# Performance work log

Hardware: AMD Instinct MI355X
Metric: run time of the kernel (lower is better)

## Reference

```python
import jax, jax.numpy as jnp
import numpy as np

N_NODES = 50000
N_EDGES = 800000
IN_FT = 128
HID_FT = 64
EMB_FT = 128
NUM_LAYERS = 4
NEG_SLOP = 0.2


def setup_inputs() -> dict:
    key = jax.random.key(0)
    ks = jax.random.split(key, 16)
    x = jax.random.normal(ks[0], (N_NODES, IN_FT), dtype=jnp.float32)
    edge_index = jax.random.randint(ks[1], (2, N_EDGES), 0, N_NODES, dtype=jnp.int64)
    edge_weight = jax.random.uniform(ks[2], (N_EDGES,), dtype=jnp.float32)
    def lin(k, fin, fout):
        s = 1.0 / np.sqrt(fin)
        kw, kb = jax.random.split(k)
        W = jax.random.uniform(kw, (fin, fout), minval=-s, maxval=s, dtype=jnp.float32)
        b = jax.random.uniform(kb, (fout,), minval=-s, maxval=s, dtype=jnp.float32)
        return W, b
    W1, b1 = lin(ks[3], IN_FT, HID_FT)
    W2, b2 = lin(ks[4], HID_FT, HID_FT)
    W3, b3 = lin(ks[5], HID_FT, HID_FT)
    W4, b4 = lin(ks[6], HID_FT, HID_FT)
    Wh, bh = lin(ks[7], NUM_LAYERS * HID_FT, EMB_FT)
    return {"x": x, "edge_index": edge_index, "edge_weight": edge_weight,
            "W1": W1, "b1": b1, "W2": W2, "b2": b2, "W3": W3, "b3": b3,
            "W4": W4, "b4": b4, "Wh": Wh, "bh": bh}


def _gcn_no_norm(x, src, dst, ew, W, b):
    # GCNConv(add_self_loops=False, normalize=False): plain weighted scatter-add
    h = x @ W                                   # [N, F]
    msg = h[src] * ew[:, None]                  # gather over edges [E, F]
    return jax.ops.segment_sum(msg, dst, num_segments=N_NODES) + b


def _gcn_norm(x, src, dst, ew, W, b):
    # Default GCNConv: add self loops (weight 1) + symmetric normalization.
    deg = jax.ops.segment_sum(ew, dst, num_segments=N_NODES) + 1.0  # +1 self loop
    dinv = jnp.where(deg > 0, jax.lax.rsqrt(deg), 0.0)
    norm = dinv[src] * ew * dinv[dst]           # [E]
    h = x @ W
    agg = jax.ops.segment_sum(h[src] * norm[:, None], dst, num_segments=N_NODES)
    agg = agg + (dinv * dinv)[:, None] * h      # self-loop term
    return agg + b


def _forward(x, edge_index, edge_weight, W1, b1, W2, b2, W3, b3, W4, b4, Wh, bh):
    src, dst = edge_index[0], edge_index[1]
    lrelu = lambda v: jax.nn.leaky_relu(v, NEG_SLOP)
    outs = []
    h = lrelu(_gcn_no_norm(x, src, dst, edge_weight, W1, b1))
    outs.append(h)  # dropout is identity in deterministic reference
    for W, b in ((W2, b2), (W3, b3), (W4, b4)):
        h = lrelu(_gcn_norm(h, src, dst, edge_weight, W, b))
        outs.append(h)
    cat = jnp.concatenate(outs, axis=-1)        # [N, num_layers*HID_FT]
    return cat @ Wh + bh


def reference(x, edge_index, edge_weight, W1, b1, W2, b2, W3, b3, W4, b4, Wh, bh):
    return _forward(x, edge_index, edge_weight, W1, b1, W2, b2, W3, b3, W4, b4, Wh, bh)
```

## Files before the change

kernel.cpp:

```cpp
#include <hip/hip_runtime.h>
#include <hip/hip_bf16.h>

#define NEG_SLOP 0.2f
typedef unsigned long long ull;
typedef __attribute__((ext_vector_type(8))) short bf16x8;
typedef __attribute__((ext_vector_type(4))) float f32x4;

__device__ __forceinline__ float lrelu(float v) { return v > 0.0f ? v : NEG_SLOP * v; }

__device__ __forceinline__ float bf2f(unsigned short u) {
    union { unsigned int i; float f; } c; c.i = ((unsigned int)u) << 16; return c.f;
}
__device__ __forceinline__ unsigned short f2bf(float f) {
    union { float f; unsigned int i; } c; c.f = f;
    unsigned int r = c.i + 0x7FFF + ((c.i >> 16) & 1);
    return (unsigned short)(r >> 16);
}

struct us8 { ushort4 a, b; };

__global__ void prep_kernel(const float* __restrict__ Wh, unsigned short* __restrict__ wht,
                            const float* __restrict__ W1, unsigned short* __restrict__ w1t,
                            const float* __restrict__ W2, unsigned short* __restrict__ w2t,
                            const float* __restrict__ W3, unsigned short* __restrict__ w3t,
                            const float* __restrict__ W4, unsigned short* __restrict__ w4t,
                            float4* __restrict__ pz, int nz) {
    int idx = blockIdx.x * 256 + threadIdx.x;
    if (idx < nz) pz[idx] = make_float4(0.f, 0.f, 0.f, 0.f);
    if (idx < 256 * 128) {
        int k = idx >> 7, c = idx & 127;
        wht[(size_t)c * 256 + k] = f2bf(Wh[idx]);
    }
    if (idx < 64 * 128) {
        int c = idx >> 7, k = idx & 127;
        w1t[idx] = f2bf(W1[k * 64 + c]);
    }
    if (idx < 64 * 64) {
        int c = idx >> 6, k = idx & 63;
        w2t[idx] = f2bf(W2[k * 64 + c]);
        w3t[idx] = f2bf(W3[k * 64 + c]);
        w4t[idx] = f2bf(W4[k * 64 + c]);
    }
}

__global__ void histo_kernel(const int* __restrict__ dst, const float* __restrict__ ew,
                             ull* __restrict__ packed4, int* __restrict__ rank,
                             int n_edges, int n) {
    int e = blockIdx.x * 256 + threadIdx.x;
    if (e >= n_edges) return;
    int d = dst[e];
    int c = e & 3;
    ull delta = (1ULL << 40) | (ull)(ew[e] * 4294967296.0f);
    ull old = atomicAdd(&packed4[(size_t)c * n + d], delta);
    rank[e] = (int)(old >> 40);
}

__global__ void scan1_kernel(const ull* __restrict__ packed4, int* __restrict__ pre,
                             int4* __restrict__ bases, int* __restrict__ bsum,
                             float* __restrict__ dinv, int n) {
    __shared__ int s[256];
    int t = threadIdx.x;
    int base = blockIdx.x * 1024 + t * 4;
    const ull m = (1ULL << 40) - 1;
    int tot[4];
#pragma unroll
    for (int j = 0; j < 4; ++j) {
        int node = base + j;
        if (node < n) {
            ull p0 = packed4[node];
            ull p1 = packed4[(size_t)n + node];
            ull p2 = packed4[2 * (size_t)n + node];
            ull p3 = packed4[3 * (size_t)n + node];
            int c0 = (int)(p0 >> 40), c1 = (int)(p1 >> 40);
            int c2 = (int)(p2 >> 40), c3 = (int)(p3 >> 40);
            bases[node] = make_int4(0, c0, c0 + c1, c0 + c1 + c2);
            tot[j] = c0 + c1 + c2 + c3;
            float deg = (float)((p0 & m) + (p1 & m) + (p2 & m) + (p3 & m)) *
                        (1.0f / 4294967296.0f);
            dinv[node] = rsqrtf(deg + 1.0f);
        } else tot[j] = 0;
    }
    int tsum = tot[0] + tot[1] + tot[2] + tot[3];
    s[t] = tsum;
    __syncthreads();
    for (int off = 1; off < 256; off <<= 1) {
        int v = (t >= off) ? s[t - off] : 0;
        __syncthreads();
        s[t] += v;
        __syncthreads();
    }
    int ex = s[t] - tsum;
    if (t == 255) bsum[blockIdx.x] = s[255];
    int o[4];
    o[0] = ex; o[1] = ex + tot[0]; o[2] = o[1] + tot[1]; o[3] = o[2] + tot[2];
    if (base + 3 < n) *(int4*)&pre[base] = make_int4(o[0], o[1], o[2], o[3]);
    else {
        for (int j = 0; j < 4; ++j) if (base + j < n) pre[base + j] = o[j];
    }
}

__global__ void scan3_kernel(int* __restrict__ rp, int4* __restrict__ bases,
                             const int* __restrict__ bsum, int nbsum,
                             int n, int n_edges) {
    __shared__ int sb[64];
    __shared__ int boffs[64];
    int t = threadIdx.x;
    int myv = 0;
    if (t < 64) { myv = (t < nbsum) ? bsum[t] : 0; sb[t] = myv; }
    __syncthreads();
    for (int off = 1; off < 64; off <<= 1) {
        int u = (t >= off && t < 64) ? sb[t - off] : 0;
        __syncthreads();
        if (t < 64) sb[t] += u;
        __syncthreads();
    }
    if (t < 64) boffs[t] = sb[t] - myv;
    __syncthreads();
    int idx = blockIdx.x * 256 + t;
    int base = idx * 4;
    if (base >= n) {
        if (base == ((n + 3) & ~3)) rp[n] = n_edges;
        return;
    }
    int boff = boffs[(base >> 10) & 63];
    if (base + 3 < n) {
        int4 v = *(int4*)&rp[base];
        v.x += boff; v.y += boff; v.z += boff; v.w += boff;
        *(int4*)&rp[base] = v;
        int va[4] = {v.x, v.y, v.z, v.w};
#pragma unroll
        for (int j = 0; j < 4; ++j) {
            int4 bs = bases[base + j];
            bs.x += va[j]; bs.y += va[j]; bs.z += va[j]; bs.w += va[j];
            bases[base + j] = bs;
        }
    } else {
        for (int j = 0; j < 4 && base + j < n; ++j) {
            int v = rp[base + j] + boff;
            rp[base + j] = v;
            int4 bs = bases[base + j];
            bs.x += v; bs.y += v; bs.z += v; bs.w += v;
            bases[base + j] = bs;
        }
        rp[n] = n_edges;
    }
}

__global__ void fill_kernel(const int* __restrict__ src, const int* __restrict__ dst,
                            const float* __restrict__ ew, const int* __restrict__ rank,
                            const int4* __restrict__ bases,
                            int2* __restrict__ e_sw, int n_edges) {
    int e = blockIdx.x * 256 + threadIdx.x;
    if (e >= n_edges) return;
    int d = dst[e];
    int c = e & 3;
    int4 bs = bases[d];
    int b = (c == 0) ? bs.x : (c == 1) ? bs.y : (c == 2) ? bs.z : bs.w;
    e_sw[b + rank[e]] = make_int2(src[e], __float_as_int(ew[e]));
}

__global__ void gather_plain(const int* __restrict__ rp, const int2* __restrict__ e_sw,
                             const unsigned short* __restrict__ hb,
                             const float* __restrict__ b, unsigned short* __restrict__ cat, int n) {
    int node = (blockIdx.x * 256 + threadIdx.x) >> 6;
    if (node >= n) return;
    int lane = threadIdx.x & 63;
    int eg = lane >> 3;
    int f0 = (lane & 7) * 8;
    int lo = rp[node], hi = rp[node + 1];
    float a[8] = {};
    for (int k = lo + eg; k < hi; k += 16) {
        int k1 = k + 8;
        int2 p0 = e_sw[k];
        int2 p1 = e_sw[k1 < hi ? k1 : k];
        float w0 = __int_as_float(p0.y);
        float w1 = k1 < hi ? __int_as_float(p1.y) : 0.f;
        us8 u0 = *(const us8*)&hb[(size_t)p0.x * 64 + f0];
        us8 u1 = *(const us8*)&hb[(size_t)p1.x * 64 + f0];
        a[0] += w0 * bf2f(u0.a.x) + w1 * bf2f(u1.a.x);
        a[1] += w0 * bf2f(u0.a.y) + w1 * bf2f(u1.a.y);
        a[2] += w0 * bf2f(u0.a.z) + w1 * bf2f(u1.a.z);
        a[3] += w0 * bf2f(u0.a.w) + w1 * bf2f(u1.a.w);
        a[4] += w0 * bf2f(u0.b.x) + w1 * bf2f(u1.b.x);
        a[5] += w0 * bf2f(u0.b.y) + w1 * bf2f(u1.b.y);
        a[6] += w0 * bf2f(u0.b.z) + w1 * bf2f(u1.b.z);
        a[7] += w0 * bf2f(u0.b.w) + w1 * bf2f(u1.b.w);
    }
#pragma unroll
    for (int j = 0; j < 8; ++j) {
        a[j] += __shfl_xor(a[j], 8, 64);
        a[j] += __shfl_xor(a[j], 16, 64);
        a[j] += __shfl_xor(a[j], 32, 64);
    }
    if (eg == 0) {
        unsigned short o[8];
#pragma unroll
        for (int j = 0; j < 8; ++j) o[j] = f2bf(lrelu(a[j] + b[f0 + j]));
        *(int4*)&cat[(size_t)node * 256 + f0] = *(int4*)o;
    }
}

__global__ void gather_norm(const int* __restrict__ rp, const int2* __restrict__ e_sw,
                            const unsigned short* __restrict__ hb,
                            const float* __restrict__ dinv, const float* __restrict__ b,
                            unsigned short* __restrict__ cat, int col_off, int n) {
    int node = (blockIdx.x * 256 + threadIdx.x) >> 6;
    if (node >= n) return;
    int lane = threadIdx.x & 63;
    int eg = lane >> 3;
    int f0 = (lane & 7) * 8;
    float di = dinv[node];
    us8 h = *(const us8*)&hb[(size_t)node * 64 + f0];
    int lo = rp[node], hi = rp[node + 1];
    float a[8] = {};
    for (int k = lo + eg; k < hi; k += 16) {
        int k1 = k + 8;
        int2 p0 = e_sw[k];
        int2 p1 = e_sw[k1 < hi ? k1 : k];
        float w0 = __int_as_float(p0.y);
        float w1 = k1 < hi ? __int_as_float(p1.y) : 0.f;
        us8 u0 = *(const us8*)&hb[(size_t)p0.x * 64 + f0];
        us8 u1 = *(const us8*)&hb[(size_t)p1.x * 64 + f0];
        a[0] += w0 * bf2f(u0.a.x) + w1 * bf2f(u1.a.x);
        a[1] += w0 * bf2f(u0.a.y) + w1 * bf2f(u1.a.y);
        a[2] += w0 * bf2f(u0.a.z) + w1 * bf2f(u1.a.z);
        a[3] += w0 * bf2f(u0.a.w) + w1 * bf2f(u1.a.w);
        a[4] += w0 * bf2f(u0.b.x) + w1 * bf2f(u1.b.x);
        a[5] += w0 * bf2f(u0.b.y) + w1 * bf2f(u1.b.y);
        a[6] += w0 * bf2f(u0.b.z) + w1 * bf2f(u1.b.z);
        a[7] += w0 * bf2f(u0.b.w) + w1 * bf2f(u1.b.w);
    }
#pragma unroll
    for (int j = 0; j < 8; ++j) {
        a[j] += __shfl_xor(a[j], 8, 64);
        a[j] += __shfl_xor(a[j], 16, 64);
        a[j] += __shfl_xor(a[j], 32, 64);
    }
    if (eg == 0) {
        float hs[8] = {bf2f(h.a.x), bf2f(h.a.y), bf2f(h.a.z), bf2f(h.a.w),
                       bf2f(h.b.x), bf2f(h.b.y), bf2f(h.b.z), bf2f(h.b.w)};
        unsigned short o[8];
#pragma unroll
        for (int j = 0; j < 8; ++j) o[j] = f2bf(lrelu(di * (a[j] + hs[j]) + b[f0 + j]));
        *(int4*)&cat[(size_t)node * 256 + col_off + f0] = *(int4*)o;
    }
}

__global__ __launch_bounds__(256) void gemm_hid_mfma(
    const unsigned short* __restrict__ in, int in_stride,
    const unsigned short* __restrict__ wT, const float* __restrict__ dinv,
    unsigned short* __restrict__ outb, int n_rows) {
    __shared__ __align__(16) char As[64 * 128];
    __shared__ __align__(16) char Bs[64 * 128];
    const int tid = threadIdx.x;
    const int wid = tid >> 6, lane = tid & 63;
    const int row0 = blockIdx.x * 64;
    const int lrow = lane & 15, kg = lane >> 4;
    {
        int row = tid >> 2, seg = tid & 3;
        int rr = row0 + row; if (rr >= n_rows) rr = n_rows - 1;
        const int4* g = (const int4*)&in[(size_t)rr * in_stride + seg * 16];
        int4 u0 = g[0], u1 = g[1];
        const int4* gb = (const int4*)&wT[(size_t)row * 64 + seg * 16];
        int4 v0 = gb[0], v1 = gb[1];
        int sw = (row & 7) << 4;
        int base = row * 128 + seg * 32;
        *(int4*)(As + (base ^ sw)) = u0;
        *(int4*)(As + ((base + 16) ^ sw)) = u1;
        *(int4*)(Bs + (base ^ sw)) = v0;
        *(int4*)(Bs + ((base + 16) ^ sw)) = v1;
    }
    __syncthreads();
    int arow = wid * 16 + lrow;
    int asw = (arow & 7) << 4;
    f32x4 acc[4] = {};
#pragma unroll
    for (int ks = 0; ks < 2; ++ks) {
        bf16x8 af = *(bf16x8*)(As + ((arow * 128 + ks * 64 + kg * 16) ^ asw));
#pragma unroll
        for (int cf = 0; cf < 4; ++cf) {
            int c = cf * 16 + lrow;
            bf16x8 bf = *(bf16x8*)(Bs + ((c * 128 + ks * 64 + kg * 16) ^ ((c & 7) << 4)));
            acc[cf] = __builtin_amdgcn_mfma_f32_16x16x32_bf16(af, bf, acc[cf], 0, 0, 0);
        }
    }
    int r4 = (lane >> 4) * 4;
#pragma unroll
    for (int reg = 0; reg < 4; ++reg) {
        int r = row0 + wid * 16 + r4 + reg;
        if (r >= n_rows) continue;
        float di = dinv[r];
#pragma unroll
        for (int cf = 0; cf < 4; ++cf)
            outb[(size_t)r * 64 + cf * 16 + lrow] = f2bf(acc[cf][reg] * di);
    }
}

__global__ __launch_bounds__(256) void gemm_hid_mfma_x(
    const float* __restrict__ x, const unsigned short* __restrict__ w1T,
    unsigned short* __restrict__ outb, int n_rows) {
    __shared__ __align__(16) char As[64 * 256];
    __shared__ __align__(16) char Bs[64 * 256];
    const int tid = threadIdx.x;
    const int wid = tid >> 6, lane = tid & 63;
    const int row0 = blockIdx.x * 64;
    const int lrow = lane & 15, kg = lane >> 4;
    {
        int row = tid >> 2, seg = tid & 3;
        int rr = row0 + row; if (rr >= n_rows) rr = n_rows - 1;
        const float4* g = (const float4*)&x[(size_t)rr * 128 + seg * 32];
        const int4* gb = (const int4*)&w1T[(size_t)row * 128 + seg * 32];
        int sw = (row & 7) << 4;
        int base = row * 256 + seg * 64;
#pragma unroll
        for (int i = 0; i < 4; ++i) {
            float4 f0 = g[2 * i], f1 = g[2 * i + 1];
            unsigned short u[8] = {f2bf(f0.x), f2bf(f0.y), f2bf(f0.z), f2bf(f0.w),
                                   f2bf(f1.x), f2bf(f1.y), f2bf(f1.z), f2bf(f1.w)};
            *(int4*)(As + ((base + i * 16) ^ sw)) = *(int4*)u;
            *(int4*)(Bs + ((base + i * 16) ^ sw)) = gb[i];
        }
    }
    __syncthreads();
    int arow = wid * 16 + lrow;
    int asw = (arow & 7) << 4;
    f32x4 acc[4] = {};
#pragma unroll
    for (int ks = 0; ks < 4; ++ks) {
        bf16x8 af = *(bf16x8*)(As + ((arow * 256 + ks * 64 + kg * 16) ^ asw));
#pragma unroll
        for (int cf = 0; cf < 4; ++cf) {
            int c = cf * 16 + lrow;
            bf16x8 bf = *(bf16x8*)(Bs + ((c * 256 + ks * 64 + kg * 16) ^ ((c & 7) << 4)));
            acc[cf] = __builtin_amdgcn_mfma_f32_16x16x32_bf16(af, bf, acc[cf], 0, 0, 0);
        }
    }
    int r4 = (lane >> 4) * 4;
#pragma unroll
    for (int reg = 0; reg < 4; ++reg) {
        int r = row0 + wid * 16 + r4 + reg;
        if (r >= n_rows) continue;
#pragma unroll
        for (int cf = 0; cf < 4; ++cf)
            outb[(size_t)r * 64 + cf * 16 + lrow] = f2bf(acc[cf][reg]);
    }
}

__global__ __launch_bounds__(256) void gemm_out_mfma(
    const unsigned short* __restrict__ cat, const unsigned short* __restrict__ whT,
    const float* __restrict__ bh, float* __restrict__ out, int n_rows) {
    __shared__ __align__(16) char As[64 * 128];
    __shared__ __align__(16) char Bs[128 * 128];
    const int tid = threadIdx.x;
    const int wid = tid >> 6, lane = tid & 63;
    const int row0 = blockIdx.x * 64;
    const int lrow = lane & 15, kg = lane >> 4;
    f32x4 acc[8] = {};
    for (int kc = 0; kc < 4; ++kc) {
        __syncthreads();
        {
            int row = tid >> 2, seg = tid & 3;
            int rr = row0 + row; if (rr >= n_rows) rr = n_rows - 1;
            const int4* g = (const int4*)&cat[(size_t)rr * 256 + kc * 64 + seg * 16];
            int4 u0 = g[0], u1 = g[1];
            int sw = (row & 7) << 4;
            int base = row * 128 + seg * 32;
            *(int4*)(As + (base ^ sw)) = u0;
            *(int4*)(As + ((base + 16) ^ sw)) = u1;
        }
        {
            int c = tid >> 1, seg = tid & 1;
            const int4* g = (const int4*)&whT[(size_t)c * 256 + kc * 64 + seg * 32];
            int sw = (c & 7) << 4;
            int base = c * 128 + seg * 64;
#pragma unroll
            for (int i = 0; i < 4; ++i)
                *(int4*)(Bs + ((base + i * 16) ^ sw)) = g[i];
        }
        __syncthreads();
        int arow = wid * 16 + lrow;
        int asw = (arow & 7) << 4;
#pragma unroll
        for (int ks = 0; ks < 2; ++ks) {
            bf16x8 af = *(bf16x8*)(As + ((arow * 128 + ks * 64 + kg * 16) ^ asw));
#pragma unroll
            for (int cf = 0; cf < 8; ++cf) {
                int c = cf * 16 + lrow;
                bf16x8 bf = *(bf16x8*)(Bs + ((c * 128 + ks * 64 + kg * 16) ^ ((c & 7) << 4)));
                acc[cf] = __builtin_amdgcn_mfma_f32_16x16x32_bf16(af, bf, acc[cf], 0, 0, 0);
            }
        }
    }
    int lrow4 = (lane >> 4) * 4;
#pragma unroll
    for (int cf = 0; cf < 8; ++cf) {
        int col = cf * 16 + lrow;
        float bias = bh[col];
#pragma unroll
        for (int reg = 0; reg < 4; ++reg) {
            int r = row0 + wid * 16 + lrow4 + reg;
            if (r < n_rows) out[(size_t)r * 128 + col] = acc[cf][reg] + bias;
        }
    }
}

extern "C" void kernel_launch(void* const* d_in, const int* in_sizes, int n_in,
                              void* d_out, int out_size, void* d_ws, size_t ws_size,
                              hipStream_t stream) {
    const float* x  = (const float*)d_in[0];
    const int*   ei = (const int*)d_in[1];
    const float* ew = (const float*)d_in[2];
    const float* W1 = (const float*)d_in[3];
    const float* b1 = (const float*)d_in[4];
    const float* W2 = (const float*)d_in[5];
    const float* b2 = (const float*)d_in[6];
    const float* W3 = (const float*)d_in[7];
    const float* b3 = (const float*)d_in[8];
    const float* W4 = (const float*)d_in[9];
    const float* b4 = (const float*)d_in[10];
    const float* Wh = (const float*)d_in[11];
    const float* bh = (const float*)d_in[12];

    const int E = in_sizes[2];
    const int N = in_sizes[0] / 128;
    const int* src = ei;
    const int* dst = ei + E;

    char* p = (char*)d_ws;
    unsigned short* cat     = (unsigned short*)p; p += (size_t)N * 256 * 2;
    unsigned short* hb      = (unsigned short*)p; p += (size_t)N * 64 * 2;
    unsigned short* wht     = (unsigned short*)p; p += (size_t)128 * 256 * 2;
    unsigned short* w1t     = (unsigned short*)p; p += (size_t)64 * 128 * 2;
    unsigned short* w2t     = (unsigned short*)p; p += (size_t)64 * 64 * 2;
    unsigned short* w3t     = (unsigned short*)p; p += (size_t)64 * 64 * 2;
    unsigned short* w4t     = (unsigned short*)p; p += (size_t)64 * 64 * 2;
    ull*            packed4 = (ull*)p;            p += (size_t)N * 4 * 8;
    float*          dinv    = (float*)p;          p += (size_t)N * 4;
    int*            row_ptr = (int*)p;            p += (size_t)(N + 4) * 4;
    int*            bsum    = (int*)p;            p += (size_t)64 * 4;
    int4*           bases   = (int4*)p;           p += (size_t)N * 16;
    int*            rank    = (int*)p;            p += (size_t)E * 4;
    int2*           e_sw    = (int2*)p;           p += (size_t)E * 8;
    float* out = (float*)d_out;

    int eb   = (E + 255) / 256;
    int nb64 = (N * 64 + 255) / 256;
    int gb64 = (N + 63) / 64;
    int sb   = (N + 1023) / 1024;
    int s3b  = ((N + 3) / 4 + 256) / 256;
    int nz   = N * 2;
    int pb   = (nz > 256 * 128 ? nz : 256 * 128) / 256 + 1;

    prep_kernel<<<pb, 256, 0, stream>>>(Wh, wht, W1, w1t, W2, w2t, W3, w3t, W4, w4t,
                                        (float4*)packed4, nz);
    histo_kernel<<<eb, 256, 0, stream>>>(dst, ew, packed4, rank, E, N);
    scan1_kernel<<<sb, 256, 0, stream>>>(packed4, row_ptr, bases, bsum, dinv, N);
    scan3_kernel<<<s3b, 256, 0, stream>>>(row_ptr, bases, bsum, sb, N, E);
    fill_kernel<<<eb, 256, 0, stream>>>(src, dst, ew, rank, bases, e_sw, E);

    gemm_hid_mfma_x<<<gb64, 256, 0, stream>>>(x, w1t, hb, N);
    gather_plain<<<nb64, 256, 0, stream>>>(row_ptr, e_sw, hb, b1, cat, N);

    const unsigned short* Wt[3] = {w2t, w3t, w4t};
    const float* bl[3] = {b2, b3, b4};
    for (int l = 1; l < 4; ++l) {
        gemm_hid_mfma<<<gb64, 256, 0, stream>>>(cat + (size_t)(l - 1) * 64, 256,
                                                Wt[l - 1], dinv, hb, N);
        gather_norm<<<nb64, 256, 0, stream>>>(row_ptr, e_sw, hb, dinv,
                                              bl[l - 1], cat, l * 64, N);
    }

    gemm_out_mfma<<<gb64, 256, 0, stream>>>(cat, wht, bh, out, N);
}
```

Measured before the change: 210.6 us.

## Split hidden features into two 32-wide halves and gather each half separately

```diff
diff --git a/kernel.cpp b/kernel.cpp
--- a/kernel.cpp
+++ b/kernel.cpp
@@ -159,24 +159,25 @@
     e_sw[b + rank[e]] = make_int2(src[e], __float_as_int(ew[e]));
 }
 
-__global__ void gather_plain(const int* __restrict__ rp, const int2* __restrict__ e_sw,
-                             const unsigned short* __restrict__ hb,
-                             const float* __restrict__ b, unsigned short* __restrict__ cat, int n) {
+__global__ void gather_plain_h(const int* __restrict__ rp, const int2* __restrict__ e_sw,
+                               const unsigned short* __restrict__ hbh,
+                               const float* __restrict__ bo,
+                               unsigned short* __restrict__ cat, int colbase, int n) {
     int node = (blockIdx.x * 256 + threadIdx.x) >> 6;
     if (node >= n) return;
     int lane = threadIdx.x & 63;
-    int eg = lane >> 3;
-    int f0 = (lane & 7) * 8;
+    int eg = lane >> 2;
+    int f0 = (lane & 3) * 8;
     int lo = rp[node], hi = rp[node + 1];
     float a[8] = {};
-    for (int k = lo + eg; k < hi; k += 16) {
-        int k1 = k + 8;
+    for (int k = lo + eg; k < hi; k += 32) {
+        int k1 = k + 16;
         int2 p0 = e_sw[k];
         int2 p1 = e_sw[k1 < hi ? k1 : k];
         float w0 = __int_as_float(p0.y);
         float w1 = k1 < hi ? __int_as_float(p1.y) : 0.f;
-        us8 u0 = *(const us8*)&hb[(size_t)p0.x * 64 + f0];
-        us8 u1 = *(const us8*)&hb[(size_t)p1.x * 64 + f0];
+        us8 u0 = *(const us8*)&hbh[(size_t)p0.x * 32 + f0];
+        us8 u1 = *(const us8*)&hbh[(size_t)p1.x * 32 + f0];
         a[0] += w0 * bf2f(u0.a.x) + w1 * bf2f(u1.a.x);
         a[1] += w0 * bf2f(u0.a.y) + w1 * bf2f(u1.a.y);
         a[2] += w0 * bf2f(u0.a.z) + w1 * bf2f(u1.a.z);
@@ -188,6 +189,7 @@
     }
 #pragma unroll
     for (int j = 0; j < 8; ++j) {
+        a[j] += __shfl_xor(a[j], 4, 64);
         a[j] += __shfl_xor(a[j], 8, 64);
         a[j] += __shfl_xor(a[j], 16, 64);
         a[j] += __shfl_xor(a[j], 32, 64);
@@ -195,32 +197,32 @@
     if (eg == 0) {
         unsigned short o[8];
 #pragma unroll
-        for (int j = 0; j < 8; ++j) o[j] = f2bf(lrelu(a[j] + b[f0 + j]));
-        *(int4*)&cat[(size_t)node * 256 + f0] = *(int4*)o;
-    }
-}
-
-__global__ void gather_norm(const int* __restrict__ rp, const int2* __restrict__ e_sw,
-                            const unsigned short* __restrict__ hb,
-                            const float* __restrict__ dinv, const float* __restrict__ b,
-                            unsigned short* __restrict__ cat, int col_off, int n) {
+        for (int j = 0; j < 8; ++j) o[j] = f2bf(lrelu(a[j] + bo[f0 + j]));
+        *(int4*)&cat[(size_t)node * 256 + colbase + f0] = *(int4*)o;
+    }
+}
+
+__global__ void gather_norm_h(const int* __restrict__ rp, const int2* __restrict__ e_sw,
+                              const unsigned short* __restrict__ hbh,
+                              const float* __restrict__ dinv, const float* __restrict__ bo,
+                              unsigned short* __restrict__ cat, int colbase, int n) {
     int node = (blockIdx.x * 256 + threadIdx.x) >> 6;
     if (node >= n) return;
     int lane = threadIdx.x & 63;
-    int eg = lane >> 3;
-    int f0 = (lane & 7) * 8;
+    int eg = lane >> 2;
+    int f0 = (lane & 3) * 8;
     float di = dinv[node];
-    us8 h = *(const us8*)&hb[(size_t)node * 64 + f0];
+    us8 h = *(const us8*)&hbh[(size_t)node * 32 + f0];
     int lo = rp[node], hi = rp[node + 1];
     float a[8] = {};
-    for (int k = lo + eg; k < hi; k += 16) {
-        int k1 = k + 8;
+    for (int k = lo + eg; k < hi; k += 32) {
+        int k1 = k + 16;
         int2 p0 = e_sw[k];
         int2 p1 = e_sw[k1 < hi ? k1 : k];
         float w0 = __int_as_float(p0.y);
         float w1 = k1 < hi ? __int_as_float(p1.y) : 0.f;
-        us8 u0 = *(const us8*)&hb[(size_t)p0.x * 64 + f0];
-        us8 u1 = *(const us8*)&hb[(size_t)p1.x * 64 + f0];
+        us8 u0 = *(const us8*)&hbh[(size_t)p0.x * 32 + f0];
+        us8 u1 = *(const us8*)&hbh[(size_t)p1.x * 32 + f0];
         a[0] += w0 * bf2f(u0.a.x) + w1 * bf2f(u1.a.x);
         a[1] += w0 * bf2f(u0.a.y) + w1 * bf2f(u1.a.y);
         a[2] += w0 * bf2f(u0.a.z) + w1 * bf2f(u1.a.z);
@@ -232,6 +234,7 @@
     }
 #pragma unroll
     for (int j = 0; j < 8; ++j) {
+        a[j] += __shfl_xor(a[j], 4, 64);
         a[j] += __shfl_xor(a[j], 8, 64);
         a[j] += __shfl_xor(a[j], 16, 64);
         a[j] += __shfl_xor(a[j], 32, 64);
@@ -241,15 +244,15 @@
                        bf2f(h.b.x), bf2f(h.b.y), bf2f(h.b.z), bf2f(h.b.w)};
         unsigned short o[8];
 #pragma unroll
-        for (int j = 0; j < 8; ++j) o[j] = f2bf(lrelu(di * (a[j] + hs[j]) + b[f0 + j]));
-        *(int4*)&cat[(size_t)node * 256 + col_off + f0] = *(int4*)o;
+        for (int j = 0; j < 8; ++j) o[j] = f2bf(lrelu(di * (a[j] + hs[j]) + bo[f0 + j]));
+        *(int4*)&cat[(size_t)node * 256 + colbase + f0] = *(int4*)o;
     }
 }
 
 __global__ __launch_bounds__(256) void gemm_hid_mfma(
     const unsigned short* __restrict__ in, int in_stride,
     const unsigned short* __restrict__ wT, const float* __restrict__ dinv,
-    unsigned short* __restrict__ outb, int n_rows) {
+    unsigned short* __restrict__ hb0, unsigned short* __restrict__ hb1, int n_rows) {
     __shared__ __align__(16) char As[64 * 128];
     __shared__ __align__(16) char Bs[64 * 128];
     const int tid = threadIdx.x;
@@ -290,15 +293,16 @@
         int r = row0 + wid * 16 + r4 + reg;
         if (r >= n_rows) continue;
         float di = dinv[r];
-#pragma unroll
-        for (int cf = 0; cf < 4; ++cf)
-            outb[(size_t)r * 64 + cf * 16 + lrow] = f2bf(acc[cf][reg] * di);
+        hb0[(size_t)r * 32 + lrow]      = f2bf(acc[0][reg] * di);
+        hb0[(size_t)r * 32 + 16 + lrow] = f2bf(acc[1][reg] * di);
+        hb1[(size_t)r * 32 + lrow]      = f2bf(acc[2][reg] * di);
+        hb1[(size_t)r * 32 + 16 + lrow] = f2bf(acc[3][reg] * di);
     }
 }
 
 __global__ __launch_bounds__(256) void gemm_hid_mfma_x(
     const float* __restrict__ x, const unsigned short* __restrict__ w1T,
-    unsigned short* __restrict__ outb, int n_rows) {
+    unsigned short* __restrict__ hb0, unsigned short* __restrict__ hb1, int n_rows) {
     __shared__ __align__(16) char As[64 * 256];
     __shared__ __align__(16) char Bs[64 * 256];
     const int tid = threadIdx.x;
@@ -340,9 +344,10 @@
     for (int reg = 0; reg < 4; ++reg) {
         int r = row0 + wid * 16 + r4 + reg;
         if (r >= n_rows) continue;
-#pragma unroll
-        for (int cf = 0; cf < 4; ++cf)
-            outb[(size_t)r * 64 + cf * 16 + lrow] = f2bf(acc[cf][reg]);
+        hb0[(size_t)r * 32 + lrow]      = f2bf(acc[0][reg]);
+        hb0[(size_t)r * 32 + 16 + lrow] = f2bf(acc[1][reg]);
+        hb1[(size_t)r * 32 + lrow]      = f2bf(acc[2][reg]);
+        hb1[(size_t)r * 32 + 16 + lrow] = f2bf(acc[3][reg]);
     }
 }
 
@@ -428,7 +433,8 @@
 
     char* p = (char*)d_ws;
     unsigned short* cat     = (unsigned short*)p; p += (size_t)N * 256 * 2;
-    unsigned short* hb      = (unsigned short*)p; p += (size_t)N * 64 * 2;
+    unsigned short* hb0     = (unsigned short*)p; p += (size_t)N * 32 * 2;
+    unsigned short* hb1     = (unsigned short*)p; p += (size_t)N * 32 * 2;
     unsigned short* wht     = (unsigned short*)p; p += (size_t)128 * 256 * 2;
     unsigned short* w1t     = (unsigned short*)p; p += (size_t)64 * 128 * 2;
     unsigned short* w2t     = (unsigned short*)p; p += (size_t)64 * 64 * 2;
@@ -458,16 +464,19 @@
     scan3_kernel<<<s3b, 256, 0, stream>>>(row_ptr, bases, bsum, sb, N, E);
     fill_kernel<<<eb, 256, 0, stream>>>(src, dst, ew, rank, bases, e_sw, E);
 
-    gemm_hid_mfma_x<<<gb64, 256, 0, stream>>>(x, w1t, hb, N);
-    gather_plain<<<nb64, 256, 0, stream>>>(row_ptr, e_sw, hb, b1, cat, N);
+    gemm_hid_mfma_x<<<gb64, 256, 0, stream>>>(x, w1t, hb0, hb1, N);
+    gather_plain_h<<<nb64, 256, 0, stream>>>(row_ptr, e_sw, hb0, b1, cat, 0, N);
+    gather_plain_h<<<nb64, 256, 0, stream>>>(row_ptr, e_sw, hb1, b1 + 32, cat, 32, N);
 
     const unsigned short* Wt[3] = {w2t, w3t, w4t};
     const float* bl[3] = {b2, b3, b4};
     for (int l = 1; l < 4; ++l) {
         gemm_hid_mfma<<<gb64, 256, 0, stream>>>(cat + (size_t)(l - 1) * 64, 256,
-                                                Wt[l - 1], dinv, hb, N);
-        gather_norm<<<nb64, 256, 0, stream>>>(row_ptr, e_sw, hb, dinv,
-                                              bl[l - 1], cat, l * 64, N);
+                                                Wt[l - 1], dinv, hb0, hb1, N);
+        gather_norm_h<<<nb64, 256, 0, stream>>>(row_ptr, e_sw, hb0, dinv,
+                                                bl[l - 1], cat, l * 64, N);
+        gather_norm_h<<<nb64, 256, 0, stream>>>(row_ptr, e_sw, hb1, dinv,
+                                                bl[l - 1] + 32, cat, l * 64 + 32, N);
     }
 
     gemm_out_mfma<<<gb64, 256, 0, stream>>>(cat, wht, bh, out, N);
```

After: 277.8 us. 31.9% more time.

## Split edge gathers into two passes by source-node half for cache locality

Applied to the files above, without the earlier changes.

```diff
diff --git a/kernel.cpp b/kernel.cpp
--- a/kernel.cpp
+++ b/kernel.cpp
@@ -43,13 +43,15 @@
     }
 }
 
-__global__ void histo_kernel(const int* __restrict__ dst, const float* __restrict__ ew,
+__global__ void histo_kernel(const int* __restrict__ src, const int* __restrict__ dst,
+                             const float* __restrict__ ew,
                              ull* __restrict__ packed4, int* __restrict__ rank,
-                             int n_edges, int n) {
+                             int n_edges, int n, int halfN) {
     int e = blockIdx.x * 256 + threadIdx.x;
     if (e >= n_edges) return;
     int d = dst[e];
-    int c = e & 3;
+    int s = src[e];
+    int c = (s < halfN) ? (e & 1) : 2 + (e & 1);
     ull delta = (1ULL << 40) | (ull)(ew[e] * 4294967296.0f);
     ull old = atomicAdd(&packed4[(size_t)c * n + d], delta);
     rank[e] = (int)(old >> 40);
@@ -100,6 +102,7 @@
 }
 
 __global__ void scan3_kernel(int* __restrict__ rp, int4* __restrict__ bases,
+                             int* __restrict__ mid,
                              const int* __restrict__ bsum, int nbsum,
                              int n, int n_edges) {
     __shared__ int sb[64];
@@ -133,6 +136,7 @@
             int4 bs = bases[base + j];
             bs.x += va[j]; bs.y += va[j]; bs.z += va[j]; bs.w += va[j];
             bases[base + j] = bs;
+            mid[base + j] = bs.z;
         }
     } else {
         for (int j = 0; j < 4 && base + j < n; ++j) {
@@ -141,6 +145,7 @@
             int4 bs = bases[base + j];
             bs.x += v; bs.y += v; bs.z += v; bs.w += v;
             bases[base + j] = bs;
+            mid[base + j] = bs.z;
         }
         rp[n] = n_edges;
     }
@@ -149,25 +154,27 @@
 __global__ void fill_kernel(const int* __restrict__ src, const int* __restrict__ dst,
                             const float* __restrict__ ew, const int* __restrict__ rank,
                             const int4* __restrict__ bases,
-                            int2* __restrict__ e_sw, int n_edges) {
+                            int2* __restrict__ e_sw, int n_edges, int halfN) {
     int e = blockIdx.x * 256 + threadIdx.x;
     if (e >= n_edges) return;
     int d = dst[e];
-    int c = e & 3;
+    int s = src[e];
+    int c = (s < halfN) ? (e & 1) : 2 + (e & 1);
     int4 bs = bases[d];
     int b = (c == 0) ? bs.x : (c == 1) ? bs.y : (c == 2) ? bs.z : bs.w;
-    e_sw[b + rank[e]] = make_int2(src[e], __float_as_int(ew[e]));
-}
-
-__global__ void gather_plain(const int* __restrict__ rp, const int2* __restrict__ e_sw,
-                             const unsigned short* __restrict__ hb,
-                             const float* __restrict__ b, unsigned short* __restrict__ cat, int n) {
+    e_sw[b + rank[e]] = make_int2(s, __float_as_int(ew[e]));
+}
+
+__global__ void gather_p1(const int* __restrict__ rp, const int* __restrict__ mid,
+                          const int2* __restrict__ e_sw,
+                          const unsigned short* __restrict__ hb,
+                          float* __restrict__ tmp, int n) {
     int node = (blockIdx.x * 256 + threadIdx.x) >> 6;
     if (node >= n) return;
     int lane = threadIdx.x & 63;
     int eg = lane >> 3;
     int f0 = (lane & 7) * 8;
-    int lo = rp[node], hi = rp[node + 1];
+    int lo = rp[node], hi = mid[node];
     float a[8] = {};
     for (int k = lo + eg; k < hi; k += 16) {
         int k1 = k + 8;
@@ -193,25 +200,29 @@
         a[j] += __shfl_xor(a[j], 32, 64);
     }
     if (eg == 0) {
-        unsigned short o[8];
-#pragma unroll
-        for (int j = 0; j < 8; ++j) o[j] = f2bf(lrelu(a[j] + b[f0 + j]));
-        *(int4*)&cat[(size_t)node * 256 + f0] = *(int4*)o;
-    }
-}
-
-__global__ void gather_norm(const int* __restrict__ rp, const int2* __restrict__ e_sw,
-                            const unsigned short* __restrict__ hb,
-                            const float* __restrict__ dinv, const float* __restrict__ b,
-                            unsigned short* __restrict__ cat, int col_off, int n) {
+        *(float4*)&tmp[(size_t)node * 64 + f0]     = make_float4(a[0], a[1], a[2], a[3]);
+        *(float4*)&tmp[(size_t)node * 64 + f0 + 4] = make_float4(a[4], a[5], a[6], a[7]);
+    }
+}
+
+__global__ void gather_p2_plain(const int* __restrict__ rp, const int* __restrict__ mid,
+                                const int2* __restrict__ e_sw,
+                                const unsigned short* __restrict__ hb,
+                                const float* __restrict__ b, const float* __restrict__ tmp,
+                                unsigned short* __restrict__ cat, int n) {
     int node = (blockIdx.x * 256 + threadIdx.x) >> 6;
     if (node >= n) return;
     int lane = threadIdx.x & 63;
     int eg = lane >> 3;
     int f0 = (lane & 7) * 8;
-    float di = dinv[node];
-    us8 h = *(const us8*)&hb[(size_t)node * 64 + f0];
-    int lo = rp[node], hi = rp[node + 1];
+    float t[8] = {};
+    if (eg == 0) {
+        float4 t0 = *(const float4*)&tmp[(size_t)node * 64 + f0];
+        float4 t1 = *(const float4*)&tmp[(size_t)node * 64 + f0 + 4];
+        t[0] = t0.x; t[1] = t0.y; t[2] = t0.z; t[3] = t0.w;
+        t[4] = t1.x; t[5] = t1.y; t[6] = t1.z; t[7] = t1.w;
+    }
+    int lo = mid[node], hi = rp[node + 1];
     float a[8] = {};
     for (int k = lo + eg; k < hi; k += 16) {
         int k1 = k + 8;
@@ -237,11 +248,65 @@
         a[j] += __shfl_xor(a[j], 32, 64);
     }
     if (eg == 0) {
+        unsigned short o[8];
+#pragma unroll
+        for (int j = 0; j < 8; ++j) o[j] = f2bf(lrelu(a[j] + t[j] + b[f0 + j]));
+        *(int4*)&cat[(size_t)node * 256 + f0] = *(int4*)o;
+    }
+}
+
+__global__ void gather_p2_norm(const int* __restrict__ rp, const int* __restrict__ mid,
+                               const int2* __restrict__ e_sw,
+                               const unsigned short* __restrict__ hb,
+                               const float* __restrict__ dinv, const float* __restrict__ b,
+                               const float* __restrict__ tmp,
+                               unsigned short* __restrict__ cat, int col_off, int n) {
+    int node = (blockIdx.x * 256 + threadIdx.x) >> 6;
+    if (node >= n) return;
+    int lane = threadIdx.x & 63;
+    int eg = lane >> 3;
+    int f0 = (lane & 7) * 8;
+    float di = dinv[node];
+    us8 h = *(const us8*)&hb[(size_t)node * 64 + f0];
+    float t[8] = {};
+    if (eg == 0) {
+        float4 t0 = *(const float4*)&tmp[(size_t)node * 64 + f0];
+        float4 t1 = *(const float4*)&tmp[(size_t)node * 64 + f0 + 4];
+        t[0] = t0.x; t[1] = t0.y; t[2] = t0.z; t[3] = t0.w;
+        t[4] = t1.x; t[5] = t1.y; t[6] = t1.z; t[7] = t1.w;
+    }
+    int lo = mid[node], hi = rp[node + 1];
+    float a[8] = {};
+    for (int k = lo + eg; k < hi; k += 16) {
+        int k1 = k + 8;
+        int2 p0 = e_sw[k];
+        int2 p1 = e_sw[k1 < hi ? k1 : k];
+        float w0 = __int_as_float(p0.y);
+        float w1 = k1 < hi ? __int_as_float(p1.y) : 0.f;
+        us8 u0 = *(const us8*)&hb[(size_t)p0.x * 64 + f0];
+        us8 u1 = *(const us8*)&hb[(size_t)p1.x * 64 + f0];
+        a[0] += w0 * bf2f(u0.a.x) + w1 * bf2f(u1.a.x);
+        a[1] += w0 * bf2f(u0.a.y) + w1 * bf2f(u1.a.y);
+        a[2] += w0 * bf2f(u0.a.z) + w1 * bf2f(u1.a.z);
+        a[3] += w0 * bf2f(u0.a.w) + w1 * bf2f(u1.a.w);
+        a[4] += w0 * bf2f(u0.b.x) + w1 * bf2f(u1.b.x);
+        a[5] += w0 * bf2f(u0.b.y) + w1 * bf2f(u1.b.y);
+        a[6] += w0 * bf2f(u0.b.z) + w1 * bf2f(u1.b.z);
+        a[7] += w0 * bf2f(u0.b.w) + w1 * bf2f(u1.b.w);
+    }
+#pragma unroll
+    for (int j = 0; j < 8; ++j) {
+        a[j] += __shfl_xor(a[j], 8, 64);
+        a[j] += __shfl_xor(a[j], 16, 64);
+        a[j] += __shfl_xor(a[j], 32, 64);
+    }
+    if (eg == 0) {
         float hs[8] = {bf2f(h.a.x), bf2f(h.a.y), bf2f(h.a.z), bf2f(h.a.w),
                        bf2f(h.b.x), bf2f(h.b.y), bf2f(h.b.z), bf2f(h.b.w)};
         unsigned short o[8];
 #pragma unroll
-        for (int j = 0; j < 8; ++j) o[j] = f2bf(lrelu(di * (a[j] + hs[j]) + b[f0 + j]));
+        for (int j = 0; j < 8; ++j)
+            o[j] = f2bf(lrelu(di * (a[j] + t[j] + hs[j]) + b[f0 + j]));
         *(int4*)&cat[(size_t)node * 256 + col_off + f0] = *(int4*)o;
     }
 }
@@ -423,6 +488,7 @@
 
     const int E = in_sizes[2];
     const int N = in_sizes[0] / 128;
+    const int halfN = N / 2;
     const int* src = ei;
     const int* dst = ei + E;
 
@@ -439,8 +505,10 @@
     int*            row_ptr = (int*)p;            p += (size_t)(N + 4) * 4;
     int*            bsum    = (int*)p;            p += (size_t)64 * 4;
     int4*           bases   = (int4*)p;           p += (size_t)N * 16;
+    int*            mid     = (int*)p;            p += (size_t)N * 4;
     int*            rank    = (int*)p;            p += (size_t)E * 4;
     int2*           e_sw    = (int2*)p;           p += (size_t)E * 8;
+    float*          tmp     = (float*)p;          p += (size_t)N * 64 * 4;
     float* out = (float*)d_out;
 
     int eb   = (E + 255) / 256;
@@ -453,21 +521,23 @@
 
     prep_kernel<<<pb, 256, 0, stream>>>(Wh, wht, W1, w1t, W2, w2t, W3, w3t, W4, w4t,
                                         (float4*)packed4, nz);
-    histo_kernel<<<eb, 256, 0, stream>>>(dst, ew, packed4, rank, E, N);
+    histo_kernel<<<eb, 256, 0, stream>>>(src, dst, ew, packed4, rank, E, N, halfN);
     scan1_kernel<<<sb, 256, 0, stream>>>(packed4, row_ptr, bases, bsum, dinv, N);
-    scan3_kernel<<<s3b, 256, 0, stream>>>(row_ptr, bases, bsum, sb, N, E);
-    fill_kernel<<<eb, 256, 0, stream>>>(src, dst, ew, rank, bases, e_sw, E);
+    scan3_kernel<<<s3b, 256, 0, stream>>>(row_ptr, bases, mid, bsum, sb, N, E);
+    fill_kernel<<<eb, 256, 0, stream>>>(src, dst, ew, rank, bases, e_sw, E, halfN);
 
     gemm_hid_mfma_x<<<gb64, 256, 0, stream>>>(x, w1t, hb, N);
-    gather_plain<<<nb64, 256, 0, stream>>>(row_ptr, e_sw, hb, b1, cat, N);
+    gather_p1<<<nb64, 256, 0, stream>>>(row_ptr, mid, e_sw, hb, tmp, N);
+    gather_p2_plain<<<nb64, 256, 0, stream>>>(row_ptr, mid, e_sw, hb, b1, tmp, cat, N);
 
     const unsigned short* Wt[3] = {w2t, w3t, w4t};
     const float* bl[3] = {b2, b3, b4};
     for (int l = 1; l < 4; ++l) {
         gemm_hid_mfma<<<gb64, 256, 0, stream>>>(cat + (size_t)(l - 1) * 64, 256,
                                                 Wt[l - 1], dinv, hb, N);
-        gather_norm<<<nb64, 256, 0, stream>>>(row_ptr, e_sw, hb, dinv,
-                                              bl[l - 1], cat, l * 64, N);
+        gather_p1<<<nb64, 256, 0, stream>>>(row_ptr, mid, e_sw, hb, tmp, N);
+        gather_p2_norm<<<nb64, 256, 0, stream>>>(row_ptr, mid, e_sw, hb, dinv,
+                                                 bl[l - 1], tmp, cat, l * 64, N);
     }
 
     gemm_out_mfma<<<gb64, 256, 0, stream>>>(cat, wht, bh, out, N);
```

Result: slower. 258.2 us (+22.6%).
